# Kernel tuning notes

Hardware: AMD Instinct MI355X
Metric: run time of the kernel (lower is better)

Reference implementation:

```python
import jax, jax.numpy as jnp
import numpy as np

NEG = -1e12  # additive causal mask value used in the original TF code


def setup_inputs() -> dict:
    key = jax.random.key(0)
    k1, k2, k3, k4 = jax.random.split(key, 4)
    B, T, D, U = 4, 4096, 128, 128
    query = jax.random.normal(k1, (B, T, D), dtype=jnp.float32)
    # glorot-style scaled dense weights (no bias, matching use_bias=False)
    s = 1.0 / np.sqrt(D)
    Wq = jax.random.normal(k2, (D, U), dtype=jnp.float32) * s
    Wk = jax.random.normal(k3, (D, U), dtype=jnp.float32) * s
    Wv = jax.random.normal(k4, (D, U), dtype=jnp.float32) * s
    return {"query": query, "Wq": Wq, "Wk": Wk, "Wv": Wv}


def reference(query, Wq, Wk, Wv):
    # Self-attention path: value = key = query (pre-projection)
    q = jnp.einsum('btd,du->btu', query, Wq)
    k = jnp.einsum('btd,du->btu', query, Wk)
    v = jnp.einsum('btd,du->btu', query, Wv)
    T = v.shape[1]
    # NOTE: original scales by sqrt(seq_len) (tf.shape(value)[1]), kept faithfully
    scores = jnp.einsum('bqu,bku->bqk', q, k) / jnp.sqrt(jnp.asarray(T, jnp.float32))
    # additive causal mask: lower-triangular kept, upper gets -1e12
    causal = jnp.tril(jnp.ones((T, T), dtype=jnp.float32))
    scores = scores + NEG * (1.0 - causal)
    attn = jax.nn.softmax(scores, axis=-1)
    context = jnp.einsum('bqk,bku->bqu', attn, v)
    return context
```

## Files before the change

### kernel.cpp

```cpp
#include <hip/hip_runtime.h>

#define T_SEQ 4096
#define BATCH 4
#define DD 128
#define BT (BATCH * T_SEQ)

typedef __bf16 bf16x8 __attribute__((ext_vector_type(8)));
typedef float f32x4 __attribute__((ext_vector_type(4)));

__device__ inline bf16x8 ld8(const unsigned short* p) {
  return *reinterpret_cast<const bf16x8*>(p);
}
__device__ inline unsigned short bfc(float f) {
  __bf16 v = (__bf16)f;
  return __builtin_bit_cast(unsigned short, v);
}

#define MFMA(a, b, c) __builtin_amdgcn_mfma_f32_16x16x32_bf16((a), (b), (c), 0, 0, 0)

__global__ void wt_kernel(const float* __restrict__ Wq, const float* __restrict__ Wk,
                          const float* __restrict__ Wv,
                          unsigned short* __restrict__ fq, unsigned short* __restrict__ fk,
                          unsigned short* __restrict__ fv) {
  const float* W = (blockIdx.y == 0) ? Wq : (blockIdx.y == 1) ? Wk : Wv;
  unsigned short* F = (blockIdx.y == 0) ? fq : (blockIdx.y == 1) ? fk : fv;
  int e = blockIdx.x * 256 + threadIdx.x;
  int j = e & 7, lane = (e >> 3) & 63, nc = e >> 9;
  int c = nc & 3, n0 = nc >> 2;
  int t = lane & 15, g = lane >> 4;
  F[e] = bfc(W[(c * 32 + g * 8 + j) * 128 + n0 * 16 + t]);
}

__global__ __launch_bounds__(256) void proj_kernel(
    const float* __restrict__ X,
    const unsigned short* __restrict__ fq,
    const unsigned short* __restrict__ fk,
    const unsigned short* __restrict__ fv,
    unsigned short* __restrict__ qf,
    unsigned short* __restrict__ kf,
    unsigned short* __restrict__ vt) {
  const int tid = threadIdx.x;
  const int w = tid >> 6, lane = tid & 63;
  const int t = lane & 15, g = lane >> 4;
  const int r0 = blockIdx.x * 32;

  __shared__ unsigned short xs[2][16 * 136];

  bf16x8 wq[2][4], wk[2][4], wv[2][4];
#pragma unroll
  for (int s = 0; s < 2; ++s)
#pragma unroll
    for (int c = 0; c < 4; ++c) {
      int fo = (((w + s * 4) * 4 + c) * 64 + lane) * 8;
      wq[s][c] = ld8(fq + fo);
      wk[s][c] = ld8(fk + fo);
      wv[s][c] = ld8(fv + fo);
    }

#pragma unroll
  for (int sub = 0; sub < 2; ++sub) {
    int r = tid >> 4, cb = tid & 15;
    const float* xp = X + (size_t)(r0 + sub * 16 + r) * DD + cb * 8;
    float4 lo = *reinterpret_cast<const float4*>(xp);
    float4 hi = *reinterpret_cast<const float4*>(xp + 4);
    bf16x8 tmp;
    tmp[0] = (__bf16)lo.x; tmp[1] = (__bf16)lo.y; tmp[2] = (__bf16)lo.z; tmp[3] = (__bf16)lo.w;
    tmp[4] = (__bf16)hi.x; tmp[5] = (__bf16)hi.y; tmp[6] = (__bf16)hi.z; tmp[7] = (__bf16)hi.w;
    *reinterpret_cast<bf16x8*>(&xs[sub][r * 136 + cb * 8]) = tmp;
  }
  __syncthreads();

#pragma unroll
  for (int sub = 0; sub < 2; ++sub) {
    const int r0s = r0 + sub * 16;
    bf16x8 x[4];
#pragma unroll
    for (int c = 0; c < 4; ++c)
      x[c] = ld8(&xs[sub][t * 136 + c * 32 + g * 8]);

#pragma unroll
    for (int s = 0; s < 2; ++s) {
      const int n0 = w + s * 4;
      f32x4 aq = {0.f, 0.f, 0.f, 0.f}, ak = {0.f, 0.f, 0.f, 0.f};
#pragma unroll
      for (int c = 0; c < 4; ++c) {
        aq = MFMA(x[c], wq[s][c], aq);
        ak = MFMA(x[c], wk[s][c], ak);
      }
      const int cP = n0 >> 1;
      const int Gp = ((n0 & 1) << 1) | (t >> 3);
      const int ep = t & 7;
#pragma unroll
      for (int r = 0; r < 4; ++r) {
        int row = r0s + g * 4 + r;
        size_t qoff = ((size_t)((row >> 4) * 4 + cP) * 64 + ((Gp << 4) | (row & 15))) * 8 + ep;
        qf[qoff] = bfc(aq[r] * 0.015625f);
        int tp = (row & 3) | (((row >> 3) & 3) << 2);
        size_t koff =
            ((size_t)(((row >> 5) * 2 + ((row >> 2) & 1)) * 4 + cP) * 64 + ((Gp << 4) | tp)) * 8 +
            ep;
        kf[koff] = bfc(ak[r]);
      }
    }

    const int key = r0s + t;
    const size_t vbase = (size_t)(key >> 5) * 4096 + (key & 31);
#pragma unroll
    for (int s = 0; s < 2; ++s) {
      const int u0 = w + s * 4;
      f32x4 av = {0.f, 0.f, 0.f, 0.f};
#pragma unroll
      for (int c = 0; c < 4; ++c)
        av = MFMA(wv[s][c], x[c], av);
#pragma unroll
      for (int r = 0; r < 4; ++r)
        vt[vbase + (size_t)(u0 * 16 + g * 4 + r) * 32] = bfc(av[r]);
    }
  }
}

__global__ __launch_bounds__(256, 2) void attn_kernel(
    const unsigned short* __restrict__ qf,
    const unsigned short* __restrict__ kf,
    const unsigned short* __restrict__ vt,
    float* __restrict__ out) {
  const int tid = threadIdx.x;
  const int w = tid >> 6, lane = tid & 63;
  const int t = lane & 15, G = lane >> 4;
  const int bi = blockIdx.x;
  const int xcd = bi & 7;
  const int b = xcd >> 1;
  const int wi = ((bi >> 3) << 1) | (xcd & 1);
  const int sigma = 127 - wi;
  const int q0 = sigma * 32;
  const int nch = sigma + 1;

  const unsigned short* kfb = kf + (size_t)b * 128 * 4096;
  const unsigned short* vtb = vt + (size_t)b * 128 * 4096;

  bf16x8 qa[2][4];
#pragma unroll
  for (int p = 0; p < 2; ++p)
#pragma unroll
    for (int c = 0; c < 4; ++c)
      qa[p][c] = ld8(qf + ((size_t)((b * 256 + 2 * sigma + p) * 4 + c) * 64 + lane) * 8);

  f32x4 O[2][8];
#pragma unroll
  for (int p = 0; p < 2; ++p)
#pragma unroll
    for (int u0 = 0; u0 < 8; ++u0) O[p][u0] = (f32x4){0.f, 0.f, 0.f, 0.f};
  float ls0 = 0.f, ls1 = 0.f;

  int j = w;
  bf16x8 kcur[8];
  if (j < nch) {
    const unsigned short* kblk = kfb + (size_t)j * 4096;
#pragma unroll
    for (int ci = 0; ci < 8; ++ci) kcur[ci] = ld8(kblk + ci * 512 + lane * 8);
  }

  for (; j < nch; j += 4) {
    const int j0 = j * 32;
    const unsigned short* vblk = vtb + (size_t)j * 4096;
    bf16x8 vcur[8];
#pragma unroll
    for (int u0 = 0; u0 < 8; ++u0) vcur[u0] = ld8(vblk + (u0 * 16 + t) * 32 + G * 8);
    bf16x8 knxt[8];
    if (j + 4 < nch) {
      const unsigned short* kb2 = kfb + (size_t)(j + 4) * 4096;
#pragma unroll
      for (int ci = 0; ci < 8; ++ci) knxt[ci] = ld8(kb2 + ci * 512 + lane * 8);
    }

    f32x4 s00 = (f32x4){0.f, 0.f, 0.f, 0.f}, s01 = (f32x4){0.f, 0.f, 0.f, 0.f};
    f32x4 s10 = (f32x4){0.f, 0.f, 0.f, 0.f}, s11 = (f32x4){0.f, 0.f, 0.f, 0.f};
#pragma unroll
    for (int c = 0; c < 4; ++c) {
      s00 = MFMA(kcur[c], qa[0][c], s00);
      s01 = MFMA(kcur[4 + c], qa[0][c], s01);
      s10 = MFMA(kcur[c], qa[1][c], s10);
      s11 = MFMA(kcur[4 + c], qa[1][c], s11);
    }

    bf16x8 pb0, pb1;
#pragma unroll
    for (int r = 0; r < 4; ++r) {
      int k0 = j0 + G * 8 + r;
      float e00 = (k0 <= q0 + t) ? __expf(s00[r]) : 0.f;
      float e01 = (k0 + 4 <= q0 + t) ? __expf(s01[r]) : 0.f;
      float e10 = (k0 <= q0 + 16 + t) ? __expf(s10[r]) : 0.f;
      float e11 = (k0 + 4 <= q0 + 16 + t) ? __expf(s11[r]) : 0.f;
      ls0 += e00 + e01;
      ls1 += e10 + e11;
      pb0[r] = (__bf16)e00; pb0[r + 4] = (__bf16)e01;
      pb1[r] = (__bf16)e10; pb1[r + 4] = (__bf16)e11;
    }

#pragma unroll
    for (int u0 = 0; u0 < 8; ++u0) {
      O[0][u0] = MFMA(pb0, vcur[u0], O[0][u0]);
      O[1][u0] = MFMA(pb1, vcur[u0], O[1][u0]);
    }
#pragma unroll
    for (int ci = 0; ci < 8; ++ci) kcur[ci] = knxt[ci];
  }

  __shared__ float cmb[3][64][66];
  if (w > 0) {
#pragma unroll
    for (int p = 0; p < 2; ++p)
#pragma unroll
      for (int u0 = 0; u0 < 8; ++u0)
        *reinterpret_cast<f32x4*>(&cmb[w - 1][lane][p * 32 + u0 * 4]) = O[p][u0];
    cmb[w - 1][lane][64] = ls0;
    cmb[w - 1][lane][65] = ls1;
  }
  __syncthreads();
  if (w == 0) {
#pragma unroll
    for (int ww = 0; ww < 3; ++ww) {
#pragma unroll
      for (int p = 0; p < 2; ++p)
#pragma unroll
        for (int u0 = 0; u0 < 8; ++u0) {
          f32x4 q4 = *reinterpret_cast<const f32x4*>(&cmb[ww][lane][p * 32 + u0 * 4]);
          O[p][u0][0] += q4[0]; O[p][u0][1] += q4[1];
          O[p][u0][2] += q4[2]; O[p][u0][3] += q4[3];
        }
      ls0 += cmb[ww][lane][64];
      ls1 += cmb[ww][lane][65];
    }
    ls0 += __shfl_xor(ls0, 16); ls0 += __shfl_xor(ls0, 32);
    ls1 += __shfl_xor(ls1, 16); ls1 += __shfl_xor(ls1, 32);
    float linv0[4], linv1[4];
#pragma unroll
    for (int r = 0; r < 4; ++r) {
      linv0[r] = 1.0f / __shfl(ls0, G * 4 + r);
      linv1[r] = 1.0f / __shfl(ls1, G * 4 + r);
    }
    float* op0 = out + ((size_t)(b * T_SEQ + q0 + G * 4)) * DD + t;
    float* op1 = op0 + (size_t)16 * DD;
#pragma unroll
    for (int u0 = 0; u0 < 8; ++u0) {
#pragma unroll
      for (int r = 0; r < 4; ++r) {
        op0[(size_t)r * DD + u0 * 16] = O[0][u0][r] * linv0[r];
        op1[(size_t)r * DD + u0 * 16] = O[1][u0][r] * linv1[r];
      }
    }
  }
}

extern "C" void kernel_launch(void* const* d_in, const int* in_sizes, int n_in,
                              void* d_out, int out_size, void* d_ws, size_t ws_size,
                              hipStream_t stream) {
  const float* X  = (const float*)d_in[0];
  const float* Wq = (const float*)d_in[1];
  const float* Wk = (const float*)d_in[2];
  const float* Wv = (const float*)d_in[3];
  float* out = (float*)d_out;

  unsigned short* qf = (unsigned short*)d_ws;
  unsigned short* kf = qf + (size_t)BT * DD;
  unsigned short* vt = kf + (size_t)BT * DD;
  unsigned short* fq = vt + (size_t)BT * DD;
  unsigned short* fk = fq + DD * DD;
  unsigned short* fv = fk + DD * DD;

  dim3 wt_grid(64, 3);
  wt_kernel<<<wt_grid, 256, 0, stream>>>(Wq, Wk, Wv, fq, fk, fv);
  proj_kernel<<<BT / 32, 256, 0, stream>>>(X, fq, fk, fv, qf, kf, vt);
  attn_kernel<<<512, 256, 0, stream>>>(qf, kf, vt, out);
}
```

Before: 112.3 us.

## Split attention key range across independent waves with atomic accumulation and normalize pass

Work is redistributed so each wave, rather than each block, handles one query tile and a chunk of up to 8 key blocks, giving a triangular enumeration of 1088 blocks with 4 independent waves each. Partial outputs and row sums go to global memory with float atomics, and a separate norm kernel divides by the accumulated sum afterward. This removes the shared-memory reduction and barrier. It also folds log2(e) into the Q scale so raw v_exp_f32 can be used, computes row sums with an MFMA against a ones vector, and skips masking on fully unmasked key blocks. The cost is two memsets, atomic traffic on the whole output, an extra kernel pass, and no K prefetch.

```diff
diff --git a/kernel.cpp b/kernel.cpp
--- a/kernel.cpp
+++ b/kernel.cpp
@@ -14,6 +14,11 @@
 __device__ inline unsigned short bfc(float f) {
   __bf16 v = (__bf16)f;
   return __builtin_bit_cast(unsigned short, v);
+}
+__device__ inline float fexp2(float x) {
+  float r;
+  asm("v_exp_f32 %0, %1" : "=v"(r) : "v"(x));
+  return r;
 }
 
 #define MFMA(a, b, c) __builtin_amdgcn_mfma_f32_16x16x32_bf16((a), (b), (c), 0, 0, 0)
@@ -94,7 +99,7 @@
       for (int r = 0; r < 4; ++r) {
         int row = r0s + g * 4 + r;
         size_t qoff = ((size_t)((row >> 4) * 4 + cP) * 64 + ((Gp << 4) | (row & 15))) * 8 + ep;
-        qf[qoff] = bfc(aq[r] * 0.015625f);
+        qf[qoff] = bfc(aq[r] * 0.0225421101f);
         int tp = (row & 3) | (((row >> 3) & 3) << 2);
         size_t koff =
             ((size_t)(((row >> 5) * 2 + ((row >> 2) & 1)) * 4 + cP) * 64 + ((Gp << 4) | tp)) * 8 +
@@ -119,137 +124,125 @@
   }
 }
 
-__global__ __launch_bounds__(256, 2) void attn_kernel(
+__global__ __launch_bounds__(256, 4) void attn_kernel(
     const unsigned short* __restrict__ qf,
     const unsigned short* __restrict__ kf,
     const unsigned short* __restrict__ vt,
+    float* __restrict__ Lp,
     float* __restrict__ out) {
   const int tid = threadIdx.x;
-  const int w = tid >> 6, lane = tid & 63;
+  const int lane = tid & 63;
   const int t = lane & 15, G = lane >> 4;
   const int bi = blockIdx.x;
   const int xcd = bi & 7;
   const int b = xcd >> 1;
-  const int wi = ((bi >> 3) << 1) | (xcd & 1);
-  const int sigma = 127 - wi;
-  const int q0 = sigma * 32;
-  const int nch = sigma + 1;
-
-  const unsigned short* kfb = kf + (size_t)b * 128 * 4096;
-  const unsigned short* vtb = vt + (size_t)b * 128 * 4096;
+  const int idx = ((bi >> 3) << 1) | (xcd & 1);
+  int tw = 1087 - (idx * 4 + (tid >> 6));
+  tw = __builtin_amdgcn_readfirstlane(tw);
+  int m = 0;
+  while (tw >= 4 * (m + 1) * (m + 2)) ++m;
+  const int off = tw - 4 * m * (m + 1);
+  const int sig = __builtin_amdgcn_readfirstlane(8 * m + off / (m + 1));
+  const int g = __builtin_amdgcn_readfirstlane(off % (m + 1));
+  const int q0 = sig * 32;
+  const int jbeg = g * 8;
+  const int jend = min(jbeg + 8, sig + 1);
+
+  const unsigned short* kfb = kf + (size_t)b * (T_SEQ * DD);
+  const unsigned short* vtb = vt + (size_t)b * (T_SEQ * DD);
 
   bf16x8 qa[2][4];
 #pragma unroll
   for (int p = 0; p < 2; ++p)
 #pragma unroll
     for (int c = 0; c < 4; ++c)
-      qa[p][c] = ld8(qf + ((size_t)((b * 256 + 2 * sigma + p) * 4 + c) * 64 + lane) * 8);
+      qa[p][c] = ld8(qf + ((size_t)((b * 256 + 2 * sig + p) * 4 + c) * 64 + lane) * 8);
+
+  bf16x8 ones;
+#pragma unroll
+  for (int e = 0; e < 8; ++e) ones[e] = (__bf16)1.0f;
 
   f32x4 O[2][8];
 #pragma unroll
   for (int p = 0; p < 2; ++p)
 #pragma unroll
     for (int u0 = 0; u0 < 8; ++u0) O[p][u0] = (f32x4){0.f, 0.f, 0.f, 0.f};
-  float ls0 = 0.f, ls1 = 0.f;
-
-  int j = w;
-  bf16x8 kcur[8];
-  if (j < nch) {
+  f32x4 lv0 = {0.f, 0.f, 0.f, 0.f}, lv1 = {0.f, 0.f, 0.f, 0.f};
+
+  for (int j = jbeg; j < jend; ++j) {
     const unsigned short* kblk = kfb + (size_t)j * 4096;
-#pragma unroll
-    for (int ci = 0; ci < 8; ++ci) kcur[ci] = ld8(kblk + ci * 512 + lane * 8);
-  }
-
-  for (; j < nch; j += 4) {
-    const int j0 = j * 32;
     const unsigned short* vblk = vtb + (size_t)j * 4096;
-    bf16x8 vcur[8];
-#pragma unroll
-    for (int u0 = 0; u0 < 8; ++u0) vcur[u0] = ld8(vblk + (u0 * 16 + t) * 32 + G * 8);
-    bf16x8 knxt[8];
-    if (j + 4 < nch) {
-      const unsigned short* kb2 = kfb + (size_t)(j + 4) * 4096;
-#pragma unroll
-      for (int ci = 0; ci < 8; ++ci) knxt[ci] = ld8(kb2 + ci * 512 + lane * 8);
-    }
-
-    f32x4 s00 = (f32x4){0.f, 0.f, 0.f, 0.f}, s01 = (f32x4){0.f, 0.f, 0.f, 0.f};
-    f32x4 s10 = (f32x4){0.f, 0.f, 0.f, 0.f}, s11 = (f32x4){0.f, 0.f, 0.f, 0.f};
+    bf16x8 kc[8], vc[8];
+#pragma unroll
+    for (int ci = 0; ci < 8; ++ci) kc[ci] = ld8(kblk + ci * 512 + lane * 8);
+#pragma unroll
+    for (int u0 = 0; u0 < 8; ++u0) vc[u0] = ld8(vblk + (u0 * 16 + t) * 32 + G * 8);
+
+    f32x4 s00 = {0.f, 0.f, 0.f, 0.f}, s01 = {0.f, 0.f, 0.f, 0.f};
+    f32x4 s10 = {0.f, 0.f, 0.f, 0.f}, s11 = {0.f, 0.f, 0.f, 0.f};
 #pragma unroll
     for (int c = 0; c < 4; ++c) {
-      s00 = MFMA(kcur[c], qa[0][c], s00);
-      s01 = MFMA(kcur[4 + c], qa[0][c], s01);
-      s10 = MFMA(kcur[c], qa[1][c], s10);
-      s11 = MFMA(kcur[4 + c], qa[1][c], s11);
+      s00 = MFMA(kc[c], qa[0][c], s00);
+      s01 = MFMA(kc[4 + c], qa[0][c], s01);
+      s10 = MFMA(kc[c], qa[1][c], s10);
+      s11 = MFMA(kc[4 + c], qa[1][c], s11);
     }
 
     bf16x8 pb0, pb1;
+    if (j < sig) {
+#pragma unroll
+      for (int r = 0; r < 4; ++r) {
+        pb0[r]     = (__bf16)fexp2(s00[r]);
+        pb0[r + 4] = (__bf16)fexp2(s01[r]);
+        pb1[r]     = (__bf16)fexp2(s10[r]);
+        pb1[r + 4] = (__bf16)fexp2(s11[r]);
+      }
+    } else {
+#pragma unroll
+      for (int r = 0; r < 4; ++r) {
+        int k0 = j * 32 + G * 8 + r;
+        float e00 = (k0 <= q0 + t) ? fexp2(s00[r]) : 0.f;
+        float e01 = (k0 + 4 <= q0 + t) ? fexp2(s01[r]) : 0.f;
+        float e10 = (k0 <= q0 + 16 + t) ? fexp2(s10[r]) : 0.f;
+        float e11 = (k0 + 4 <= q0 + 16 + t) ? fexp2(s11[r]) : 0.f;
+        pb0[r] = (__bf16)e00; pb0[r + 4] = (__bf16)e01;
+        pb1[r] = (__bf16)e10; pb1[r + 4] = (__bf16)e11;
+      }
+    }
+
+    lv0 = MFMA(pb0, ones, lv0);
+    lv1 = MFMA(pb1, ones, lv1);
+#pragma unroll
+    for (int u0 = 0; u0 < 8; ++u0) {
+      O[0][u0] = MFMA(pb0, vc[u0], O[0][u0]);
+      O[1][u0] = MFMA(pb1, vc[u0], O[1][u0]);
+    }
+  }
+
+  if (t == 0) {
 #pragma unroll
     for (int r = 0; r < 4; ++r) {
-      int k0 = j0 + G * 8 + r;
-      float e00 = (k0 <= q0 + t) ? __expf(s00[r]) : 0.f;
-      float e01 = (k0 + 4 <= q0 + t) ? __expf(s01[r]) : 0.f;
-      float e10 = (k0 <= q0 + 16 + t) ? __expf(s10[r]) : 0.f;
-      float e11 = (k0 + 4 <= q0 + 16 + t) ? __expf(s11[r]) : 0.f;
-      ls0 += e00 + e01;
-      ls1 += e10 + e11;
-      pb0[r] = (__bf16)e00; pb0[r + 4] = (__bf16)e01;
-      pb1[r] = (__bf16)e10; pb1[r + 4] = (__bf16)e11;
-    }
-
-#pragma unroll
-    for (int u0 = 0; u0 < 8; ++u0) {
-      O[0][u0] = MFMA(pb0, vcur[u0], O[0][u0]);
-      O[1][u0] = MFMA(pb1, vcur[u0], O[1][u0]);
-    }
-#pragma unroll
-    for (int ci = 0; ci < 8; ++ci) kcur[ci] = knxt[ci];
-  }
-
-  __shared__ float cmb[3][64][66];
-  if (w > 0) {
-#pragma unroll
-    for (int p = 0; p < 2; ++p)
-#pragma unroll
-      for (int u0 = 0; u0 < 8; ++u0)
-        *reinterpret_cast<f32x4*>(&cmb[w - 1][lane][p * 32 + u0 * 4]) = O[p][u0];
-    cmb[w - 1][lane][64] = ls0;
-    cmb[w - 1][lane][65] = ls1;
-  }
-  __syncthreads();
-  if (w == 0) {
-#pragma unroll
-    for (int ww = 0; ww < 3; ++ww) {
-#pragma unroll
-      for (int p = 0; p < 2; ++p)
-#pragma unroll
-        for (int u0 = 0; u0 < 8; ++u0) {
-          f32x4 q4 = *reinterpret_cast<const f32x4*>(&cmb[ww][lane][p * 32 + u0 * 4]);
-          O[p][u0][0] += q4[0]; O[p][u0][1] += q4[1];
-          O[p][u0][2] += q4[2]; O[p][u0][3] += q4[3];
-        }
-      ls0 += cmb[ww][lane][64];
-      ls1 += cmb[ww][lane][65];
-    }
-    ls0 += __shfl_xor(ls0, 16); ls0 += __shfl_xor(ls0, 32);
-    ls1 += __shfl_xor(ls1, 16); ls1 += __shfl_xor(ls1, 32);
-    float linv0[4], linv1[4];
+      atomicAdd(&Lp[b * T_SEQ + q0 + G * 4 + r], lv0[r]);
+      atomicAdd(&Lp[b * T_SEQ + q0 + 16 + G * 4 + r], lv1[r]);
+    }
+  }
+  float* ob = out + ((size_t)(b * T_SEQ + q0 + G * 4)) * DD + t;
+#pragma unroll
+  for (int u0 = 0; u0 < 8; ++u0)
 #pragma unroll
     for (int r = 0; r < 4; ++r) {
-      linv0[r] = 1.0f / __shfl(ls0, G * 4 + r);
-      linv1[r] = 1.0f / __shfl(ls1, G * 4 + r);
-    }
-    float* op0 = out + ((size_t)(b * T_SEQ + q0 + G * 4)) * DD + t;
-    float* op1 = op0 + (size_t)16 * DD;
-#pragma unroll
-    for (int u0 = 0; u0 < 8; ++u0) {
-#pragma unroll
-      for (int r = 0; r < 4; ++r) {
-        op0[(size_t)r * DD + u0 * 16] = O[0][u0][r] * linv0[r];
-        op1[(size_t)r * DD + u0 * 16] = O[1][u0][r] * linv1[r];
-      }
-    }
-  }
+      atomicAdd(ob + (size_t)r * DD + u0 * 16, O[0][u0][r]);
+      atomicAdd(ob + (size_t)(16 + r) * DD + u0 * 16, O[1][u0][r]);
+    }
+}
+
+__global__ __launch_bounds__(256) void norm_kernel(float* __restrict__ out,
+                                                   const float* __restrict__ Lp) {
+  const int i = blockIdx.x * 256 + threadIdx.x;
+  float4 v = reinterpret_cast<float4*>(out)[i];
+  const float linv = 1.0f / Lp[i >> 5];
+  v.x *= linv; v.y *= linv; v.z *= linv; v.w *= linv;
+  reinterpret_cast<float4*>(out)[i] = v;
 }
 
 extern "C" void kernel_launch(void* const* d_in, const int* in_sizes, int n_in,
@@ -267,9 +260,14 @@
   unsigned short* fq = vt + (size_t)BT * DD;
   unsigned short* fk = fq + DD * DD;
   unsigned short* fv = fk + DD * DD;
+  float* Lp = (float*)(fv + DD * DD);
+
+  hipMemsetAsync(d_out, 0, (size_t)BT * DD * sizeof(float), stream);
+  hipMemsetAsync(Lp, 0, (size_t)BT * sizeof(float), stream);
 
   dim3 wt_grid(64, 3);
   wt_kernel<<<wt_grid, 256, 0, stream>>>(Wq, Wk, Wv, fq, fk, fv);
   proj_kernel<<<BT / 32, 256, 0, stream>>>(X, fq, fk, fv, qf, kf, vt);
-  attn_kernel<<<512, 256, 0, stream>>>(qf, kf, vt, out);
-}
+  attn_kernel<<<1088, 256, 0, stream>>>(qf, kf, vt, Lp, out);
+  norm_kernel<<<(BT * DD / 4) / 256, 256, 0, stream>>>(out, Lp);
+}
```

Measured after the change: 221.5 us. 1.97x slower.
